# Performance work log

Hardware: AMD Instinct MI355X
Metric: run time of the kernel (lower is better)

## Reference

```python
import jax, jax.numpy as jnp
import numpy as np

H = 2048
EPS = 1e-5

def _layernorm(x, g, b):
    mu = jnp.mean(x, axis=-1, keepdims=True)
    var = jnp.mean(jnp.square(x - mu), axis=-1, keepdims=True)
    return (x - mu) * jax.lax.rsqrt(var + EPS) * g + b

def setup_inputs() -> dict:
    key = jax.random.key(0)
    ks = jax.random.split(key, 12)
    s = 1.0 / np.sqrt(H)
    inp = {
        "x": jax.random.normal(ks[0], (2, 2048, H), dtype=jnp.float32),
        "ln1_g": jnp.ones((H,), jnp.float32),
        "ln1_b": jnp.zeros((H,), jnp.float32),
        "ln2_g": jnp.ones((H,), jnp.float32),
        "ln2_b": jnp.zeros((H,), jnp.float32),
        "qkv_w": jax.random.uniform(ks[1], (H, 3 * H), jnp.float32, -s, s),
        "qkv_b": jax.random.uniform(ks[2], (3 * H,), jnp.float32, -s, s),
        "out_w": jax.random.uniform(ks[3], (H, H), jnp.float32, -s, s),
        "out_b": jax.random.uniform(ks[4], (H,), jnp.float32, -s, s),
        "mlp_w1": jax.random.uniform(ks[5], (H, 4 * H), jnp.float32, -s, s),
        "mlp_b1": jax.random.uniform(ks[6], (4 * H,), jnp.float32, -s, s),
        "mlp_w2": jax.random.uniform(ks[7], (4 * H, H), jnp.float32, -1.0 / np.sqrt(4 * H), 1.0 / np.sqrt(4 * H)),
        "mlp_b2": jax.random.uniform(ks[8], (H,), jnp.float32, -1.0 / np.sqrt(4 * H), 1.0 / np.sqrt(4 * H)),
    }
    return inp

def reference(x, ln1_g, ln1_b, ln2_g, ln2_b, qkv_w, qkv_b, out_w, out_b, mlp_w1, mlp_b1, mlp_w2, mlp_b2):
    residual = x
    h = _layernorm(x, ln1_g, ln1_b)
    qkv = h @ qkv_w + qkv_b                      # [B,S,3H]
    q, k, v = jnp.split(qkv, 3, axis=-1)         # each [B,S,H] (single-head attention)
    scores = jnp.einsum('bsh,bth->bst', q, k) / jnp.sqrt(jnp.float32(H))
    attn = jax.nn.softmax(scores, axis=-1)
    attn_out = jnp.einsum('bst,bth->bsh', attn, v)
    attn_out = attn_out @ out_w + out_b
    x = residual + attn_out                      # dropout is identity in eval
    residual = x
    h = _layernorm(x, ln2_g, ln2_b)
    h = jax.nn.gelu(h @ mlp_w1 + mlp_b1, approximate=False)
    h = h @ mlp_w2 + mlp_b2
    return residual + h
```

## Files before the change

### kernel.cpp

```cpp
#include <hip/hip_runtime.h>
#include <hip/hip_bf16.h>
#include <math.h>

typedef __bf16 bf16_t;
typedef __bf16 bf16x8 __attribute__((ext_vector_type(8)));
typedef __bf16 bf16x4 __attribute__((ext_vector_type(4)));
typedef float  f32x4  __attribute__((ext_vector_type(4)));

enum { EPI_BF16_BIAS = 0, EPI_F32_SCALE = 1, EPI_BF16 = 2, EPI_F32_BIAS_RES = 3, EPI_BF16_BIAS_GELU = 4 };

__device__ __forceinline__ float gelu_exact(float v) {
  return 0.5f * v * (1.0f + erff(v * 0.7071067811865476f));
}

__device__ __forceinline__ void gld_lds16(const bf16_t* g, bf16_t* l) {
  __builtin_amdgcn_global_load_lds(
      (const __attribute__((address_space(1))) uint32_t*)(uintptr_t)g,
      (__attribute__((address_space(3))) uint32_t*)(uintptr_t)l, 16, 0, 0);
}

#define SB()    __builtin_amdgcn_s_barrier()
#define SCHED() __builtin_amdgcn_sched_barrier(0)
#define VMW0()  asm volatile("s_waitcnt vmcnt(0)" ::: "memory")

template<int EPI, int ZDIV>
__global__ __launch_bounds__(512, 2) void tb_gemm8(
    const bf16_t* __restrict__ A, int lda, long long strideA, long long kofA,
    const bf16_t* __restrict__ B, int ldb, long long strideB, long long kofB,
    const float* __restrict__ bias,
    const float* __restrict__ resid,
    void* __restrict__ Cp, int ldc, long long strideC,
    int K, float scale)
{
  __shared__ __align__(16) bf16_t sm[65536];

  const int tid = threadIdx.x;
  const int lane = tid & 63;
  const int wid = tid >> 6;
  const int wm = wid >> 2;
  const int wn = wid & 3;
  const int lr = lane & 15;
  const int lg = lane >> 4;
  const int z = blockIdx.z;
  const int batch = z / ZDIV;
  const int ks = z % ZDIV;
  const int m0 = blockIdx.y * 256;
  const int n0 = blockIdx.x * 256;

  const bf16_t* Ag = A + (size_t)batch * strideA + (size_t)ks * kofA + (size_t)m0 * lda;
  const bf16_t* Bg = B + (size_t)batch * strideB + (size_t)ks * kofB + (size_t)n0 * ldb;

  const int l3 = lane >> 3;
  const int sl8 = ((lane & 7) ^ l3) << 3;

  f32x4 acc[8][4];
#pragma unroll
  for (int i = 0; i < 8; ++i)
#pragma unroll
    for (int j = 0; j < 4; ++j) acc[i][j] = (f32x4){0.f, 0.f, 0.f, 0.f};

  auto stage = [&](int par, int kt) {
    bf16_t* da = sm + (par << 15);
    bf16_t* db = da + 16384;
#pragma unroll
    for (int h = 0; h < 2; ++h)
#pragma unroll
      for (int q = 0; q < 2; ++q) {
        int c = (wid << 1) + q;
        int row = (h << 7) + (c << 3) + l3;
        gld_lds16(Ag + (size_t)row * lda + kt + sl8, da + (h << 13) + (c << 9) + lane * 8);
        gld_lds16(Bg + (size_t)row * ldb + kt + sl8, db + (h << 13) + (c << 9) + lane * 8);
      }
  };

#define RD(base, rowbase, kslot) \
  (*(const bf16x8*)((base) + ((rowbase) + lr) * 64 + (((((kslot) << 2) | lg)) ^ (lr & 7)) * 8))

  const int NT = K >> 6;
  stage(0, 0);
  VMW0();
  SB();

  for (int t = 0; t < NT; ++t) {
    SCHED();
    const bf16_t* cura = sm + ((t & 1) << 15);
    const bf16_t* curb = cura + 16384;
    if (t + 1 < NT) stage((t + 1) & 1, (t + 1) << 6);

    bf16x8 bF[4][2], aF[4][2];
#pragma unroll
    for (int jj = 0; jj < 4; ++jj) {
      bF[jj][0] = RD(curb, jj * 64 + wn * 16, 0);
      bF[jj][1] = RD(curb, jj * 64 + wn * 16, 1);
    }
#pragma unroll
    for (int ii = 0; ii < 4; ++ii) {
      aF[ii][0] = RD(cura, ii * 32 + wm * 16, 0);
      aF[ii][1] = RD(cura, ii * 32 + wm * 16, 1);
    }
    __builtin_amdgcn_s_setprio(1);
#pragma unroll
    for (int ii = 0; ii < 4; ++ii)
#pragma unroll
      for (int jj = 0; jj < 4; ++jj)
#pragma unroll
        for (int kk = 0; kk < 2; ++kk)
          acc[ii][jj] = __builtin_amdgcn_mfma_f32_16x16x32_bf16(aF[ii][kk], bF[jj][kk], acc[ii][jj], 0, 0, 0);
    __builtin_amdgcn_s_setprio(0);
#pragma unroll
    for (int ii = 0; ii < 4; ++ii) {
      aF[ii][0] = RD(cura, 128 + ii * 32 + wm * 16, 0);
      aF[ii][1] = RD(cura, 128 + ii * 32 + wm * 16, 1);
    }
    __builtin_amdgcn_s_setprio(1);
#pragma unroll
    for (int ii = 0; ii < 4; ++ii)
#pragma unroll
      for (int jj = 0; jj < 4; ++jj)
#pragma unroll
        for (int kk = 0; kk < 2; ++kk)
          acc[4 + ii][jj] = __builtin_amdgcn_mfma_f32_16x16x32_bf16(aF[ii][kk], bF[jj][kk], acc[4 + ii][jj], 0, 0, 0);
    __builtin_amdgcn_s_setprio(0);

    SCHED();
    if (t + 1 < NT) {
      VMW0();
      SB();
    }
  }
#undef RD

#pragma unroll
  for (int i = 0; i < 8; ++i) {
    const int mr = ((i >> 2) << 7) + ((i & 3) << 5) + (wm << 4);
#pragma unroll
    for (int j = 0; j < 4; ++j) {
      const int nc = j * 64 + (wn << 4);
#pragma unroll
      for (int r = 0; r < 4; ++r) {
        int row = m0 + mr + lg * 4 + r;
        int col = n0 + nc + lr;
        float v = acc[i][j][r] * scale;
        if constexpr (EPI == EPI_BF16_BIAS || EPI == EPI_F32_BIAS_RES || EPI == EPI_BF16_BIAS_GELU)
          v += bias[col];
        if constexpr (EPI == EPI_BF16_BIAS_GELU)
          v = gelu_exact(v);
        if constexpr (EPI == EPI_F32_BIAS_RES)
          v += resid[(size_t)row * ldc + col];
        if constexpr (EPI == EPI_BF16_BIAS || EPI == EPI_BF16 || EPI == EPI_BF16_BIAS_GELU) {
          ((bf16_t*)Cp)[(size_t)z * strideC + (size_t)row * ldc + col] = (bf16_t)v;
        } else {
          ((float*)Cp)[(size_t)z * strideC + (size_t)row * ldc + col] = v;
        }
      }
    }
  }
}

__device__ __forceinline__ void prep_transpose(
    const float* __restrict__ in, bf16_t* __restrict__ outT, int R, int C,
    int tile_id, float (*tile)[33], int t)
{
  int tx = tile_id % (C / 32);
  int ty = tile_id / (C / 32);
  int c0 = tx * 32;
  int r0 = ty * 32;
  int r = t >> 3;
  int c4 = (t & 7) * 4;
  float4 d = *(const float4*)(in + (size_t)(r0 + r) * C + c0 + c4);
  tile[r][c4 + 0] = d.x; tile[r][c4 + 1] = d.y; tile[r][c4 + 2] = d.z; tile[r][c4 + 3] = d.w;
  __syncthreads();
  int c = t >> 3;
  int r4 = (t & 7) * 4;
  bf16x4 o;
  o[0] = (bf16_t)tile[r4 + 0][c];
  o[1] = (bf16_t)tile[r4 + 1][c];
  o[2] = (bf16_t)tile[r4 + 2][c];
  o[3] = (bf16_t)tile[r4 + 3][c];
  *(bf16x4*)(outT + (size_t)(c0 + c) * R + r0 + r4) = o;
}

__global__ __launch_bounds__(256) void tb_prep(
    const float* __restrict__ x, const float* __restrict__ g, const float* __restrict__ b,
    bf16_t* __restrict__ h,
    const float* __restrict__ qkv_w, bf16_t* __restrict__ qkv_wT,
    const float* __restrict__ out_w, bf16_t* __restrict__ out_wT,
    const float* __restrict__ w1, bf16_t* __restrict__ w1T,
    const float* __restrict__ w2, bf16_t* __restrict__ w2T)
{
  __shared__ float tile[32][33];
  __shared__ float sa[4], sb[4];
  int bid = blockIdx.x;
  int t = threadIdx.x;
  if (bid < 12288) {
    prep_transpose(qkv_w, qkv_wT, 2048, 6144, bid, tile, t);
  } else if (bid < 16384) {
    prep_transpose(out_w, out_wT, 2048, 2048, bid - 12288, tile, t);
  } else if (bid < 32768) {
    prep_transpose(w1, w1T, 2048, 8192, bid - 16384, tile, t);
  } else if (bid < 49152) {
    prep_transpose(w2, w2T, 8192, 2048, bid - 32768, tile, t);
  } else {
    int row = bid - 49152;
    const float* xr = x + (size_t)row * 2048;
    float4 v0 = *(const float4*)(xr + t * 8);
    float4 v1 = *(const float4*)(xr + t * 8 + 4);
    float a[8] = {v0.x, v0.y, v0.z, v0.w, v1.x, v1.y, v1.z, v1.w};
    float s = 0.f, q = 0.f;
#pragma unroll
    for (int j = 0; j < 8; ++j) { s += a[j]; q += a[j] * a[j]; }
#pragma unroll
    for (int o = 32; o; o >>= 1) { s += __shfl_down(s, o); q += __shfl_down(q, o); }
    int w = t >> 6, l = t & 63;
    if (l == 0) { sa[w] = s; sb[w] = q; }
    __syncthreads();
    if (t == 0) {
      sa[0] = sa[0] + sa[1] + sa[2] + sa[3];
      sb[0] = sb[0] + sb[1] + sb[2] + sb[3];
    }
    __syncthreads();
    float mu = sa[0] * (1.0f / 2048.0f);
    float var = sb[0] * (1.0f / 2048.0f) - mu * mu;
    float rs = rsqrtf(var + 1e-5f);
    float4 g0 = *(const float4*)(g + t * 8);
    float4 g1 = *(const float4*)(g + t * 8 + 4);
    float4 b0 = *(const float4*)(b + t * 8);
    float4 b1 = *(const float4*)(b + t * 8 + 4);
    float gv[8] = {g0.x, g0.y, g0.z, g0.w, g1.x, g1.y, g1.z, g1.w};
    float bv[8] = {b0.x, b0.y, b0.z, b0.w, b1.x, b1.y, b1.z, b1.w};
    bf16x8 o8;
#pragma unroll
    for (int j = 0; j < 8; ++j) o8[j] = (bf16_t)((a[j] - mu) * rs * gv[j] + bv[j]);
    *(bf16x8*)(h + (size_t)row * 2048 + t * 8) = o8;
  }
}

__global__ __launch_bounds__(256) void tb_combine_f(
    const float* __restrict__ x2, const bf16_t* __restrict__ p,
    const float* __restrict__ bias, float* __restrict__ out)
{
  size_t o = ((size_t)blockIdx.x * 256 + threadIdx.x) * 8;
  float4 a0 = *(const float4*)(x2 + o);
  float4 a1 = *(const float4*)(x2 + o + 4);
  bf16x8 pa = *(const bf16x8*)(p + o);
  bf16x8 pb = *(const bf16x8*)(p + 8388608 + o);
  size_t c = o & 2047;
  float4 b0 = *(const float4*)(bias + c);
  float4 b1 = *(const float4*)(bias + c + 4);
  float4 r0, r1;
  r0.x = a0.x + (float)pa[0] + (float)pb[0] + b0.x;
  r0.y = a0.y + (float)pa[1] + (float)pb[1] + b0.y;
  r0.z = a0.z + (float)pa[2] + (float)pb[2] + b0.z;
  r0.w = a0.w + (float)pa[3] + (float)pb[3] + b0.w;
  r1.x = a1.x + (float)pa[4] + (float)pb[4] + b1.x;
  r1.y = a1.y + (float)pa[5] + (float)pb[5] + b1.y;
  r1.z = a1.z + (float)pa[6] + (float)pb[6] + b1.z;
  r1.w = a1.w + (float)pa[7] + (float)pb[7] + b1.w;
  *(float4*)(out + o) = r0;
  *(float4*)(out + o + 4) = r1;
}

__global__ __launch_bounds__(256) void tb_combine_pv(
    const bf16_t* __restrict__ p, bf16_t* __restrict__ ao)
{
  size_t o = ((size_t)blockIdx.x * 256 + threadIdx.x) * 8;
  size_t b = o >> 22;
  size_t w = o & 4194303;
  const bf16_t* p0 = p + (b << 1) * 4194304 + w;
  const bf16_t* p1 = p0 + 4194304;
  bf16x8 a = *(const bf16x8*)p0;
  bf16x8 c = *(const bf16x8*)p1;
  bf16x8 r;
#pragma unroll
  for (int j = 0; j < 8; ++j) r[j] = (bf16_t)((float)a[j] + (float)c[j]);
  *(bf16x8*)(ao + o) = r;
}

__global__ __launch_bounds__(256) void tb_combine_ln(
    const float* __restrict__ x, const bf16_t* __restrict__ p,
    const float* __restrict__ ob,
    const float* __restrict__ g, const float* __restrict__ b,
    float* __restrict__ x2, bf16_t* __restrict__ h)
{
  __shared__ float sa[4], sb[4];
  int row = blockIdx.x;
  int t = threadIdx.x;
  const float* xr = x + (size_t)row * 2048;
  const bf16_t* p0 = p + (size_t)row * 2048;
  const bf16_t* p1 = p0 + 8388608;
  float4 v0 = *(const float4*)(xr + t * 8);
  float4 v1 = *(const float4*)(xr + t * 8 + 4);
  bf16x8 pa = *(const bf16x8*)(p0 + t * 8);
  bf16x8 pb = *(const bf16x8*)(p1 + t * 8);
  float4 o0 = *(const float4*)(ob + t * 8);
  float4 o1 = *(const float4*)(ob + t * 8 + 4);
  float a[8] = {v0.x, v0.y, v0.z, v0.w, v1.x, v1.y, v1.z, v1.w};
  float ov[8] = {o0.x, o0.y, o0.z, o0.w, o1.x, o1.y, o1.z, o1.w};
  float s = 0.f, q = 0.f;
#pragma unroll
  for (int j = 0; j < 8; ++j) {
    a[j] += (float)pa[j] + (float)pb[j] + ov[j];
    s += a[j]; q += a[j] * a[j];
  }
  float4 w0 = {a[0], a[1], a[2], a[3]};
  float4 w1 = {a[4], a[5], a[6], a[7]};
  *(float4*)(x2 + (size_t)row * 2048 + t * 8) = w0;
  *(float4*)(x2 + (size_t)row * 2048 + t * 8 + 4) = w1;
#pragma unroll
  for (int o = 32; o; o >>= 1) { s += __shfl_down(s, o); q += __shfl_down(q, o); }
  int w = t >> 6, l = t & 63;
  if (l == 0) { sa[w] = s; sb[w] = q; }
  __syncthreads();
  if (t == 0) {
    sa[0] = sa[0] + sa[1] + sa[2] + sa[3];
    sb[0] = sb[0] + sb[1] + sb[2] + sb[3];
  }
  __syncthreads();
  float mu = sa[0] * (1.0f / 2048.0f);
  float var = sb[0] * (1.0f / 2048.0f) - mu * mu;
  float rs = rsqrtf(var + 1e-5f);
  float4 g0 = *(const float4*)(g + t * 8);
  float4 g1 = *(const float4*)(g + t * 8 + 4);
  float4 b0 = *(const float4*)(b + t * 8);
  float4 b1 = *(const float4*)(b + t * 8 + 4);
  float gv[8] = {g0.x, g0.y, g0.z, g0.w, g1.x, g1.y, g1.z, g1.w};
  float bv[8] = {b0.x, b0.y, b0.z, b0.w, b1.x, b1.y, b1.z, b1.w};
  bf16x8 o8;
#pragma unroll
  for (int j = 0; j < 8; ++j) o8[j] = (bf16_t)((a[j] - mu) * rs * gv[j] + bv[j]);
  *(bf16x8*)(h + (size_t)row * 2048 + t * 8) = o8;
}

__global__ __launch_bounds__(256) void tb_transpose_bf16(
    const bf16_t* __restrict__ in, int ldin, long long sIn,
    bf16_t* __restrict__ out, int ldout, long long sOut)
{
  __shared__ bf16_t tile[32][40];
  int z = blockIdx.z;
  const bf16_t* src = in + (size_t)z * sIn;
  bf16_t* dst = out + (size_t)z * sOut;
  int c0 = blockIdx.x * 32;
  int r0 = blockIdx.y * 32;
  int t = threadIdx.x;
  int r = t >> 3;
  int c4 = (t & 7) * 4;
  bf16x4 d = *(const bf16x4*)(src + (size_t)(r0 + r) * ldin + c0 + c4);
  *(bf16x4*)&tile[r][c4] = d;
  __syncthreads();
  int c = t >> 3;
  int r4 = (t & 7) * 4;
  bf16x4 o;
  o[0] = tile[r4 + 0][c];
  o[1] = tile[r4 + 1][c];
  o[2] = tile[r4 + 2][c];
  o[3] = tile[r4 + 3][c];
  *(bf16x4*)(dst + (size_t)(c0 + c) * ldout + r0 + r4) = o;
}

__global__ __launch_bounds__(256) void tb_softmax_add(
    const bf16_t* __restrict__ p, bf16_t* __restrict__ P)
{
  __shared__ float sa[4];
  int row = blockIdx.x;
  int t = threadIdx.x;
  size_t base = ((size_t)(row >> 11) * 2) * 4194304 + (size_t)(row & 2047) * 2048;
  const bf16_t* p0 = p + base;
  const bf16_t* p1 = p0 + 4194304;
  bf16x8 a = *(const bf16x8*)(p0 + t * 8);
  bf16x8 c = *(const bf16x8*)(p1 + t * 8);
  float v[8];
#pragma unroll
  for (int j = 0; j < 8; ++j) v[j] = (float)a[j] + (float)c[j];
  float m = v[0];
#pragma unroll
  for (int j = 1; j < 8; ++j) m = fmaxf(m, v[j]);
#pragma unroll
  for (int o = 32; o; o >>= 1) m = fmaxf(m, __shfl_down(m, o));
  int w = t >> 6, l = t & 63;
  if (l == 0) sa[w] = m;
  __syncthreads();
  if (t == 0) sa[0] = fmaxf(fmaxf(sa[0], sa[1]), fmaxf(sa[2], sa[3]));
  __syncthreads();
  m = sa[0];
  __syncthreads();
  float s = 0.f;
#pragma unroll
  for (int j = 0; j < 8; ++j) { v[j] = expf(v[j] - m); s += v[j]; }
#pragma unroll
  for (int o = 32; o; o >>= 1) s += __shfl_down(s, o);
  if (l == 0) sa[w] = s;
  __syncthreads();
  if (t == 0) sa[0] = sa[0] + sa[1] + sa[2] + sa[3];
  __syncthreads();
  float inv = 1.0f / sa[0];
  bf16x8 o8;
#pragma unroll
  for (int j = 0; j < 8; ++j) o8[j] = (bf16_t)(v[j] * inv);
  *(bf16x8*)(P + (size_t)row * 2048 + t * 8) = o8;
}

extern "C" void kernel_launch(void* const* d_in, const int* in_sizes, int n_in,
                              void* d_out, int out_size, void* d_ws, size_t ws_size,
                              hipStream_t stream) {
  const float* x     = (const float*)d_in[0];
  const float* ln1_g = (const float*)d_in[1];
  const float* ln1_b = (const float*)d_in[2];
  const float* ln2_g = (const float*)d_in[3];
  const float* ln2_b = (const float*)d_in[4];
  const float* qkv_w = (const float*)d_in[5];
  const float* qkv_b = (const float*)d_in[6];
  const float* out_w = (const float*)d_in[7];
  const float* out_b = (const float*)d_in[8];
  const float* w1    = (const float*)d_in[9];
  const float* b1    = (const float*)d_in[10];
  const float* w2    = (const float*)d_in[11];
  const float* b2    = (const float*)d_in[12];
  float* out = (float*)d_out;
  char* ws = (char*)d_ws;

  bf16_t* spb    = (bf16_t*)(ws + 0);
  bf16_t* qkv_wT = (bf16_t*)(ws + 0);
  bf16_t* out_wT = (bf16_t*)(ws + 67108864);
  bf16_t* w1T    = (bf16_t*)(ws + 75497472);
  bf16_t* w2T    = (bf16_t*)(ws + 109051904);
  bf16_t* h_bf   = (bf16_t*)(ws + 142606336);
  bf16_t* qkv_bf = (bf16_t*)(ws + 159383552);
  bf16_t* mid_bf = (bf16_t*)(ws + 159383552);
  bf16_t* attn_bf= (bf16_t*)(ws + 209715200);
  bf16_t* Vt     = (bf16_t*)(ws + 226492416);
  bf16_t* ao_bf  = (bf16_t*)(ws + 243269632);
  float*  x2     = (float*)(ws + 226492416);

  const float inv_sqrt_h = 0.022097086912079608f;

  tb_prep<<<53248, 256, 0, stream>>>(
      x, ln1_g, ln1_b, h_bf,
      qkv_w, qkv_wT, out_w, out_wT, w1, w1T, w2, w2T);

  tb_gemm8<EPI_BF16_BIAS, 1><<<dim3(24, 16, 1), 512, 0, stream>>>(
      h_bf, 2048, 0, 0, qkv_wT, 2048, 0, 0, qkv_b, nullptr, qkv_bf, 6144, 0, 2048, 1.0f);

  tb_transpose_bf16<<<dim3(64, 64, 2), 256, 0, stream>>>(
      qkv_bf + 4096, 6144, 2048LL * 6144, Vt, 2048, 2048LL * 2048);

  tb_gemm8<EPI_BF16, 2><<<dim3(8, 8, 4), 512, 0, stream>>>(
      qkv_bf, 6144, 2048LL * 6144, 1024, qkv_bf + 2048, 6144, 2048LL * 6144, 1024,
      nullptr, nullptr, spb, 2048, 4194304LL, 1024, inv_sqrt_h);

  tb_softmax_add<<<4096, 256, 0, stream>>>(spb, attn_bf);

  tb_gemm8<EPI_BF16, 2><<<dim3(8, 8, 4), 512, 0, stream>>>(
      attn_bf, 2048, 2048LL * 2048, 1024, Vt, 2048, 2048LL * 2048, 1024,
      nullptr, nullptr, spb, 2048, 4194304LL, 1024, 1.0f);

  tb_combine_pv<<<4096, 256, 0, stream>>>(spb, ao_bf);

  tb_gemm8<EPI_BF16, 2><<<dim3(8, 16, 2), 512, 0, stream>>>(
      ao_bf, 2048, 0, 1024, out_wT, 2048, 0, 1024,
      nullptr, nullptr, spb, 2048, 8388608LL, 1024, 1.0f);

  tb_combine_ln<<<4096, 256, 0, stream>>>(x, spb, out_b, ln2_g, ln2_b, x2, h_bf);

  tb_gemm8<EPI_BF16_BIAS_GELU, 1><<<dim3(32, 16, 1), 512, 0, stream>>>(
      h_bf, 2048, 0, 0, w1T, 2048, 0, 0, b1, nullptr, mid_bf, 8192, 0, 2048, 1.0f);

  tb_gemm8<EPI_BF16, 2><<<dim3(8, 16, 2), 512, 0, stream>>>(
      mid_bf, 8192, 0, 4096, w2T, 8192, 0, 4096,
      nullptr, nullptr, spb, 2048, 8388608LL, 4096, 1.0f);

  tb_combine_f<<<4096, 256, 0, stream>>>(x2, spb, b2, out);
}
```

Before: 645.5 us.

## Add ping-pong quarter-pipelined GEMM variant for the MLP up-projection

```diff
diff --git a/kernel.cpp b/kernel.cpp
--- a/kernel.cpp
+++ b/kernel.cpp
@@ -22,6 +22,11 @@
 #define SB()    __builtin_amdgcn_s_barrier()
 #define SCHED() __builtin_amdgcn_sched_barrier(0)
 #define VMW0()  asm volatile("s_waitcnt vmcnt(0)" ::: "memory")
+#define VMW(N)  asm volatile("s_waitcnt vmcnt(" #N ")" ::: "memory")
+#define LGKM0() do { asm volatile("s_waitcnt lgkmcnt(0)" ::: "memory"); __builtin_amdgcn_sched_barrier(0); } while(0)
+
+#define RD(base, rowbase, kslot) \
+  (*(const bf16x8*)((base) + ((rowbase) + lr) * 64 + (((((kslot) << 2) | lg)) ^ (lr & 7)) * 8))
 
 template<int EPI, int ZDIV>
 __global__ __launch_bounds__(512, 2) void tb_gemm8(
@@ -73,9 +78,6 @@
       }
   };
 
-#define RD(base, rowbase, kslot) \
-  (*(const bf16x8*)((base) + ((rowbase) + lr) * 64 + (((((kslot) << 2) | lg)) ^ (lr & 7)) * 8))
-
   const int NT = K >> 6;
   stage(0, 0);
   VMW0();
@@ -128,7 +130,162 @@
       SB();
     }
   }
-#undef RD
+
+#pragma unroll
+  for (int i = 0; i < 8; ++i) {
+    const int mr = ((i >> 2) << 7) + ((i & 3) << 5) + (wm << 4);
+#pragma unroll
+    for (int j = 0; j < 4; ++j) {
+      const int nc = j * 64 + (wn << 4);
+#pragma unroll
+      for (int r = 0; r < 4; ++r) {
+        int row = m0 + mr + lg * 4 + r;
+        int col = n0 + nc + lr;
+        float v = acc[i][j][r] * scale;
+        if constexpr (EPI == EPI_BF16_BIAS || EPI == EPI_F32_BIAS_RES || EPI == EPI_BF16_BIAS_GELU)
+          v += bias[col];
+        if constexpr (EPI == EPI_BF16_BIAS_GELU)
+          v = gelu_exact(v);
+        if constexpr (EPI == EPI_F32_BIAS_RES)
+          v += resid[(size_t)row * ldc + col];
+        if constexpr (EPI == EPI_BF16_BIAS || EPI == EPI_BF16 || EPI == EPI_BF16_BIAS_GELU) {
+          ((bf16_t*)Cp)[(size_t)z * strideC + (size_t)row * ldc + col] = (bf16_t)v;
+        } else {
+          ((float*)Cp)[(size_t)z * strideC + (size_t)row * ldc + col] = v;
+        }
+      }
+    }
+  }
+}
+
+template<int EPI, int ZDIV>
+__global__ __launch_bounds__(512, 2) void tb_gemm8p(
+    const bf16_t* __restrict__ A, int lda, long long strideA, long long kofA,
+    const bf16_t* __restrict__ B, int ldb, long long strideB, long long kofB,
+    const float* __restrict__ bias,
+    const float* __restrict__ resid,
+    void* __restrict__ Cp, int ldc, long long strideC,
+    int K, float scale)
+{
+  __shared__ __align__(16) bf16_t sm[65536];
+
+  const int tid = threadIdx.x;
+  const int lane = tid & 63;
+  const int wid = tid >> 6;
+  const int wm = wid >> 2;
+  const int wn = wid & 3;
+  const int lr = lane & 15;
+  const int lg = lane >> 4;
+  const int z = blockIdx.z;
+  const int batch = z / ZDIV;
+  const int ks = z % ZDIV;
+  const int m0 = blockIdx.y * 256;
+  const int n0 = blockIdx.x * 256;
+
+  const bf16_t* Ag = A + (size_t)batch * strideA + (size_t)ks * kofA + (size_t)m0 * lda;
+  const bf16_t* Bg = B + (size_t)batch * strideB + (size_t)ks * kofB + (size_t)n0 * ldb;
+
+  const int l3 = lane >> 3;
+  const int sl8 = ((lane & 7) ^ l3) << 3;
+
+  f32x4 acc[8][4];
+#pragma unroll
+  for (int i = 0; i < 8; ++i)
+#pragma unroll
+    for (int j = 0; j < 4; ++j) acc[i][j] = (f32x4){0.f, 0.f, 0.f, 0.f};
+
+  auto stageU = [&](bf16_t* buf, int moff, const bf16_t* G, int ld, int h, int kt) {
+#pragma unroll
+    for (int q = 0; q < 2; ++q) {
+      int c = (wid << 1) + q;
+      int row = (h << 7) + (c << 3) + l3;
+      gld_lds16(G + (size_t)row * ld + kt + sl8, buf + moff + (h << 13) + (c << 9) + lane * 8);
+    }
+  };
+
+#define MFMA_Q(IB, JB) do { \
+  __builtin_amdgcn_s_setprio(1); \
+  _Pragma("unroll") for (int ii = 0; ii < 4; ++ii) \
+  _Pragma("unroll") for (int jj = 0; jj < 2; ++jj) \
+  _Pragma("unroll") for (int kk = 0; kk < 2; ++kk) \
+    acc[(IB)+ii][(JB)+jj] = __builtin_amdgcn_mfma_f32_16x16x32_bf16( \
+        aF[ii][kk], bF[jj][kk], acc[(IB)+ii][(JB)+jj], 0, 0, 0); \
+  __builtin_amdgcn_s_setprio(0); } while (0)
+
+  const int NT = K >> 6;
+  bf16_t* buf0 = sm;
+  bf16_t* buf1 = sm + 32768;
+
+  stageU(buf0, 0,     Ag, lda, 0, 0);
+  stageU(buf0, 16384, Bg, ldb, 0, 0);
+  stageU(buf0, 16384, Bg, ldb, 1, 0);
+  stageU(buf0, 0,     Ag, lda, 1, 0);
+  stageU(buf1, 16384, Bg, ldb, 0, 64);
+  stageU(buf1, 0,     Ag, lda, 1, 64);
+  VMW(4);
+  SB();
+
+  bf16x8 aF[4][2], bF[2][2];
+
+  for (int t = 0; t < NT; ++t) {
+    bf16_t* cur = sm + ((t & 1) << 15);
+    bf16_t* oth = sm + (((t + 1) & 1) << 15);
+    const bf16_t* curb = cur + 16384;
+    const int kt1 = (t + 1) << 6;
+    const int kt2 = (t + 2) << 6;
+
+#pragma unroll
+    for (int ii = 0; ii < 4; ++ii) {
+      aF[ii][0] = RD(cur, ii * 32 + wm * 16, 0);
+      aF[ii][1] = RD(cur, ii * 32 + wm * 16, 1);
+    }
+#pragma unroll
+    for (int jj = 0; jj < 2; ++jj) {
+      bF[jj][0] = RD(curb, jj * 64 + wn * 16, 0);
+      bF[jj][1] = RD(curb, jj * 64 + wn * 16, 1);
+    }
+    if (t + 1 < NT) stageU(oth, 0, Ag, lda, 0, kt1);
+    asm volatile("s_waitcnt lgkmcnt(8)" ::: "memory");
+    SB(); LGKM0();
+    MFMA_Q(0, 0);
+    SB();
+
+#pragma unroll
+    for (int ii = 0; ii < 4; ++ii) {
+      aF[ii][0] = RD(cur, 128 + ii * 32 + wm * 16, 0);
+      aF[ii][1] = RD(cur, 128 + ii * 32 + wm * 16, 1);
+    }
+    if (t + 1 < NT) stageU(oth, 16384, Bg, ldb, 1, kt1);
+    SB(); LGKM0();
+    MFMA_Q(4, 0);
+    SB();
+
+#pragma unroll
+    for (int jj = 0; jj < 2; ++jj) {
+      bF[jj][0] = RD(curb, 128 + jj * 64 + wn * 16, 0);
+      bF[jj][1] = RD(curb, 128 + jj * 64 + wn * 16, 1);
+    }
+    if (t + 2 < NT) stageU(cur, 16384, Bg, ldb, 0, kt2);
+    SB(); LGKM0();
+    MFMA_Q(4, 2);
+    SB();
+
+#pragma unroll
+    for (int ii = 0; ii < 4; ++ii) {
+      aF[ii][0] = RD(cur, ii * 32 + wm * 16, 0);
+      aF[ii][1] = RD(cur, ii * 32 + wm * 16, 1);
+    }
+    if (t + 2 < NT) {
+      stageU(cur, 0, Ag, lda, 1, kt2);
+      VMW(4);
+    } else if (t + 1 < NT) {
+      VMW(0);
+    }
+    SB(); LGKM0();
+    MFMA_Q(0, 2);
+    SB();
+  }
+#undef MFMA_Q
 
 #pragma unroll
   for (int i = 0; i < 8; ++i) {
@@ -461,7 +618,7 @@
 
   tb_combine_ln<<<4096, 256, 0, stream>>>(x, spb, out_b, ln2_g, ln2_b, x2, h_bf);
 
-  tb_gemm8<EPI_BF16_BIAS_GELU, 1><<<dim3(32, 16, 1), 512, 0, stream>>>(
+  tb_gemm8p<EPI_BF16_BIAS_GELU, 1><<<dim3(32, 16, 1), 512, 0, stream>>>(
       h_bf, 2048, 0, 0, w1T, 2048, 0, 0, b1, nullptr, mid_bf, 8192, 0, 2048, 1.0f);
 
   tb_gemm8<EPI_BF16, 2><<<dim3(8, 16, 2), 512, 0, stream>>>(
```

After: 656.7 us. Within noise of the previous version (+1.7%).
